# Kernel optimization log

Hardware: AMD Instinct MI355X
Metric: run time of the kernel (lower is better)

## Reference

```python
import jax, jax.numpy as jnp
import numpy as np

N = 50000          # neuron_count
NNZ = 1_600_000    # edges (avg degree 32)
B = 32             # batch
L = 3              # CONNECTOME_LAYER_NUMBER


def setup_inputs() -> dict:
    key = jax.random.key(0)
    k1, k2, k3, k4, k5 = jax.random.split(key, 5)
    x = jax.random.normal(k1, (B, N), dtype=jnp.float32)
    adj_vals = jax.random.uniform(k2, (NNZ,), dtype=jnp.float32)
    w_vals = jax.random.uniform(k3, (NNZ,), dtype=jnp.float32)
    bias = jnp.ones((N,), dtype=jnp.float32)
    row = jax.random.randint(k4, (NNZ,), 0, N, dtype=jnp.int32)
    col = jax.random.randint(k5, (NNZ,), 0, N, dtype=jnp.int32)
    return {"x": x, "adj_vals": adj_vals, "w_vals": w_vals, "bias": bias,
            "row": row, "col": col}


def _spmm(vals, row, col, dense, n):
    # (sparse NxN) @ dense [N, B] via gather + segment_sum scatter
    contrib = vals[:, None] * dense[col]          # [nnz, B]
    return jax.ops.segment_sum(contrib, row, num_segments=n)


def reference(x, adj_vals, w_vals, bias, row, col):
    # Original per layer: x = ((A @ W) @ x^T)^T + bias.
    # We use associativity: (A @ W) @ x^T == A @ (W @ x^T), avoiding the
    # explicit SpGEMM while computing the same linear map.
    n = bias.shape[0]
    xt = x.T                                      # [N, B]
    for _ in range(L):
        wx = _spmm(w_vals, row, col, xt, n)       # W @ x^T -> [N, B]
        xt = _spmm(adj_vals, row, col, wx, n)     # A @ (W @ x^T)
        xt = xt + bias[:, None]                   # broadcast bias over batch
    return xt.T                                   # [B, N]
```

## Files before the change

kernel.cpp:

```cpp
#include <hip/hip_runtime.h>


#define NN 50000
#define NNZ_E 1600000
#define NB (NN * 32)
#define CHUNK 6144
#define NBLK1 ((NNZ_E + CHUNK - 1) / CHUNK)
#define NBIN ((NN + 127) / 128)
#define NH (NBIN * NBLK1)
#define CAP2 5120
#define BCAP 6144
#define LENP (NBIN * BCAP)
#define SCAN_NBLK ((NH + 255) / 256)
#define TIN_BLKS 98

__device__ __forceinline__ int clampi(int v, int hi) {
    v = v < 0 ? 0 : v;
    return v > hi ? hi : v;
}

__device__ __forceinline__ unsigned short f2h(float v) {
    union { _Float16 h; unsigned short u; } cv;
    cv.h = (_Float16)v;
    return cv.u;
}

__device__ __forceinline__ float kv_val(unsigned kv) {
    union { unsigned short u; _Float16 h; } cv;
    cv.u = (unsigned short)(kv >> 16);
    return (float)cv.h;
}

__global__ __launch_bounds__(256) void hist_kernel(const int* __restrict__ row,
                                                   int* __restrict__ hist1,
                                                   const float* __restrict__ x,
                                                   _Float16* __restrict__ xt) {
    __shared__ int h[NBIN];
    int blk = blockIdx.x, tid = threadIdx.x;
    if (blk >= NBLK1) {
        for (int i = (blk - NBLK1) * 256 + tid; i < NB; i += TIN_BLKS * 256) {
            int n = i >> 5;
            int b = i & 31;
            xt[i] = (_Float16)x[b * NN + n];
        }
        return;
    }
    for (int j = tid; j < NBIN; j += 256) h[j] = 0;
    __syncthreads();
    int base = blk * CHUNK;
    int n = NNZ_E - base; if (n > CHUNK) n = CHUNK;
    for (int i = tid; i < n; i += 256)
        atomicAdd(&h[clampi(row[base + i], NN - 1) >> 7], 1);
    __syncthreads();
    for (int j = tid; j < NBIN; j += 256) hist1[j * NBLK1 + blk] = h[j];
}

__global__ void scan_local_kernel(int* __restrict__ data, int n, int* __restrict__ bsum) {
    __shared__ int s[256];
    int i = blockIdx.x * 256 + threadIdx.x;
    int v = (i < n) ? data[i] : 0;
    s[threadIdx.x] = v;
    __syncthreads();
    for (int off = 1; off < 256; off <<= 1) {
        int t = (threadIdx.x >= off) ? s[threadIdx.x - off] : 0;
        __syncthreads();
        s[threadIdx.x] += t;
        __syncthreads();
    }
    if (i < n) data[i] = s[threadIdx.x] - v;
    if (threadIdx.x == 255) bsum[blockIdx.x] = s[threadIdx.x];
}

__global__ __launch_bounds__(256) void scanfin_kernel(int* __restrict__ data, int n,
                                                      const int* __restrict__ bsum, int m,
                                                      int* __restrict__ binstart) {
    __shared__ int sa[512];
    __shared__ int sb[512];
    int tid = threadIdx.x;
    sa[tid]       = (tid < m) ? bsum[tid] : 0;
    sa[tid + 256] = (tid + 256 < m) ? bsum[tid + 256] : 0;
    __syncthreads();
    int* src = sa;
    int* dst = sb;
    for (int off = 1; off < 512; off <<= 1) {
#pragma unroll
        for (int q = 0; q < 2; ++q) {
            int p = tid + q * 256;
            int v = src[p];
            if (p >= off) v += src[p - off];
            dst[p] = v;
        }
        __syncthreads();
        int* t = src; src = dst; dst = t;
    }
    int add = (blockIdx.x > 0) ? src[blockIdx.x - 1] : 0;
    int i = blockIdx.x * 256 + tid;
    if (i < n) {
        int v = data[i] + add;
        data[i] = v;
        if (i % NBLK1 == 0) binstart[i / NBLK1] = v;
    }
    if (i == 0) binstart[NBIN] = NNZ_E;
}

__global__ __launch_bounds__(256) void pass1_kernel(
        const int* __restrict__ row, const int* __restrict__ col,
        const float* __restrict__ a, const float* __restrict__ w,
        const int* __restrict__ hist1_off,
        unsigned* __restrict__ k1, unsigned* __restrict__ aw1) {
    __shared__ int h[NBIN];
    __shared__ int hscan[NBIN];
    __shared__ int hoff[NBIN];
    __shared__ int s256[256];
    __shared__ unsigned sKey[CHUNK];
    __shared__ unsigned sAW[CHUNK];
    int blk = blockIdx.x, tid = threadIdx.x;
    int base = blk * CHUNK;
    int n = NNZ_E - base; if (n > CHUNK) n = CHUNK;

    for (int j = tid; j < NBIN; j += 256) {
        h[j] = 0;
        hoff[j] = hist1_off[j * NBLK1 + blk];
    }
    __syncthreads();
    for (int i = tid; i < n; i += 256)
        atomicAdd(&h[clampi(row[base + i], NN - 1) >> 7], 1);
    __syncthreads();
    int j0 = tid * 2, j1 = tid * 2 + 1;
    int c0 = (j0 < NBIN) ? h[j0] : 0;
    int c1 = (j1 < NBIN) ? h[j1] : 0;
    int tsum = c0 + c1;
    s256[tid] = tsum;
    __syncthreads();
    for (int off = 1; off < 256; off <<= 1) {
        int t = (tid >= off) ? s256[tid - off] : 0;
        __syncthreads();
        s256[tid] += t;
        __syncthreads();
    }
    int ex = s256[tid] - tsum;
    __syncthreads();
    if (j0 < NBIN) { hscan[j0] = ex;      h[j0] = ex; }
    if (j1 < NBIN) { hscan[j1] = ex + c0; h[j1] = ex + c0; }
    __syncthreads();
    for (int i = tid; i < n; i += 256) {
        int r = clampi(row[base + i], NN - 1);
        int c = clampi(col[base + i], NN - 1);
        int bin = r >> 7;
        int p = atomicAdd(&h[bin], 1);
        p = clampi(p, n - 1);
        sKey[p] = ((unsigned)r << 16) | (unsigned)c;
        sAW[p] = ((unsigned)f2h(a[base + i]) << 16) | (unsigned)f2h(w[base + i]);
    }
    __syncthreads();
    for (int p = tid; p < n; p += 256) {
        unsigned key = sKey[p];
        int bin = (int)(key >> 23);
        int d = clampi(hoff[bin] + (p - hscan[bin]), NNZ_E - 1);
        k1[d] = key;
        aw1[d] = sAW[p];
    }
}

__global__ __launch_bounds__(256) void pass2_kernel(
        const unsigned* __restrict__ k1, const unsigned* __restrict__ aw1,
        const int* __restrict__ binstart,
        unsigned* __restrict__ kvA2, unsigned* __restrict__ kvW2,
        unsigned* __restrict__ row_desc) {
    __shared__ unsigned sKey[CAP2];
    __shared__ unsigned sAW[CAP2];
    __shared__ int rh[128];
    __shared__ int rs[128];
    __shared__ int cur[128];
    int bin = blockIdx.x, tid = threadIdx.x;
    int r0 = bin << 7;
    int rows = NN - r0; if (rows > 128) rows = 128;
    int base = clampi(binstart[bin], NNZ_E);
    int size = clampi(binstart[bin + 1], NNZ_E) - base;
    size = clampi(size, CAP2);
    int pbase = bin * BCAP;

    if (tid < 128) rh[tid] = 0;
    __syncthreads();
    for (int i = tid; i < size; i += 256) {
        unsigned key = k1[base + i];
        atomicAdd(&rh[(key >> 16) & 127], 1);
        sKey[i] = key;
        sAW[i] = aw1[base + i];
    }
    __syncthreads();
    int cnt  = (tid < 128) ? rh[tid] : 0;
    int plen = (cnt + 7) & ~7;
    if (tid < 128) rs[tid] = plen;
    __syncthreads();
    for (int off = 1; off < 128; off <<= 1) {
        int t = (tid >= off && tid < 128) ? rs[tid - off] : 0;
        __syncthreads();
        if (tid < 128) rs[tid] += t;
        __syncthreads();
    }
    int rofs = (tid < 128) ? clampi(rs[tid] - plen, BCAP - 8) : 0;
    if (tid < 128) cur[tid] = rofs;
    if (tid < rows)
        row_desc[r0 + tid] = (unsigned)(pbase + rofs) | ((unsigned)(plen >> 3) << 24);
    __syncthreads();
    for (int i = tid; i < size; i += 256) {
        unsigned key = sKey[i];
        unsigned aw  = sAW[i];
        int rl = (key >> 16) & 127;
        int p = atomicAdd(&cur[rl], 1);
        p = clampi(p, BCAP - 1);
        unsigned c = key & 0xFFFFu;
        kvA2[pbase + p] = (aw & 0xFFFF0000u) | c;
        kvW2[pbase + p] = (aw << 16) | c;
    }
    __syncthreads();
    if (tid < rows) {
        int pl = (rh[tid] + 7) & ~7;
        for (int q = rh[tid]; q < pl; ++q) {
            int d = clampi(rofs + q, BCAP - 1);
            kvA2[pbase + d] = 0u;
            kvW2[pbase + d] = 0u;
        }
    }
}

template <int WITH_BIAS, int FINAL>
__global__ __launch_bounds__(256) void spmm_kernel(
        const uint2* __restrict__ kv2, const unsigned* __restrict__ row_desc,
        const unsigned* __restrict__ in32, unsigned* __restrict__ out32,
        const float* __restrict__ bias, float outScale, float biasScale,
        float* __restrict__ outf) {
    int t = blockIdx.x * 256 + threadIdx.x;
    int r = t >> 4;
    int l = t & 15;
    if (r >= NN) return;
    unsigned d = row_desc[r];
    int niter = (int)(d >> 24);
    int base2 = clampi((int)(d & 0xFFFFFFu), LENP - 8) >> 1;
    float accL = 0.0f, accH = 0.0f;
    uint2 k2[4];
    if (niter > 0) {
#pragma unroll
        for (int q = 0; q < 4; ++q) k2[q] = kv2[base2 + q];
    }
    for (int it = 0; it < niter; ++it) {
        unsigned k[8];
#pragma unroll
        for (int q = 0; q < 4; ++q) { k[2 * q] = k2[q].x; k[2 * q + 1] = k2[q].y; }
        unsigned gd[8];
#pragma unroll
        for (int j = 0; j < 8; ++j) gd[j] = in32[((k[j] & 0xFFFFu) << 4) + l];
        if (it + 1 < niter) {
            int nb2 = base2 + (it + 1) * 4;
#pragma unroll
            for (int q = 0; q < 4; ++q) k2[q] = kv2[nb2 + q];
        }
#pragma unroll
        for (int j = 0; j < 8; ++j) {
            float v = kv_val(k[j]);
            union { unsigned u; _Float16 h[2]; } cv;
            cv.u = gd[j];
            accL += v * (float)cv.h[0];
            accH += v * (float)cv.h[1];
        }
    }
    float rL = accL * outScale, rH = accH * outScale;
    if (WITH_BIAS) {
        float bb = bias[r] * biasScale;
        rL += bb; rH += bb;
    }
    if (FINAL) {
        outf[(2 * l) * NN + r]     = rL * 16777216.0f;
        outf[(2 * l + 1) * NN + r] = rH * 16777216.0f;
    } else {
        union { unsigned u; _Float16 h[2]; } o;
        o.h[0] = (_Float16)rL;
        o.h[1] = (_Float16)rH;
        out32[(r << 4) + l] = o.u;
    }
}

extern "C" void kernel_launch(void* const* d_in, const int* in_sizes, int n_in,
                              void* d_out, int out_size, void* d_ws, size_t ws_size,
                              hipStream_t stream) {
    const float* x        = (const float*)d_in[0];
    const float* adj_vals = (const float*)d_in[1];
    const float* w_vals   = (const float*)d_in[2];
    const float* bias     = (const float*)d_in[3];
    const int*   row      = (const int*)d_in[4];
    const int*   col      = (const int*)d_in[5];
    float* out = (float*)d_out;

    unsigned*  k1        = (unsigned*)d_ws;
    unsigned*  aw1       = k1 + NNZ_E;
    unsigned*  kvA2      = aw1 + NNZ_E;
    unsigned*  kvW2      = kvA2 + LENP;
    _Float16*  xt16      = (_Float16*)(kvW2 + LENP);
    _Float16*  tmp16     = xt16 + NB;
    int*   hist1         = (int*)(tmp16 + NB);
    int*   bsumB         = hist1 + NH;
    int*   binstart      = bsumB + 512;
    unsigned* row_desc   = (unsigned*)(binstart + NBIN + 8);

    const int BS = 256;
    const int grid_spmm = (NN * 16 + BS - 1) / BS;

    hist_kernel<<<NBLK1 + TIN_BLKS, BS, 0, stream>>>(row, hist1, x, xt16);
    scan_local_kernel<<<SCAN_NBLK, BS, 0, stream>>>(hist1, NH, bsumB);
    scanfin_kernel<<<SCAN_NBLK, BS, 0, stream>>>(hist1, NH, bsumB, SCAN_NBLK, binstart);

    pass1_kernel<<<NBLK1, BS, 0, stream>>>(row, col, adj_vals, w_vals,
                                           hist1, k1, aw1);
    pass2_kernel<<<NBIN, BS, 0, stream>>>(k1, aw1, binstart, kvA2, kvW2, row_desc);

    const uint2* kvA = (const uint2*)kvA2;
    const uint2* kvW = (const uint2*)kvW2;
    const unsigned* xt32  = (const unsigned*)xt16;
    unsigned*       xt32w = (unsigned*)xt16;
    const unsigned* tm32  = (const unsigned*)tmp16;
    unsigned*       tm32w = (unsigned*)tmp16;

    const float r256 = 1.0f / 256.0f;
    spmm_kernel<0, 0><<<grid_spmm, BS, 0, stream>>>(kvW, row_desc, xt32, tm32w,
                                                    nullptr, 1.0f, 0.0f, nullptr);
    spmm_kernel<1, 0><<<grid_spmm, BS, 0, stream>>>(kvA, row_desc, tm32, xt32w,
                                                    bias, r256, 1.0f / 256.0f, nullptr);
    spmm_kernel<0, 0><<<grid_spmm, BS, 0, stream>>>(kvW, row_desc, xt32, tm32w,
                                                    nullptr, 1.0f, 0.0f, nullptr);
    spmm_kernel<1, 0><<<grid_spmm, BS, 0, stream>>>(kvA, row_desc, tm32, xt32w,
                                                    bias, r256, 1.0f / 65536.0f, nullptr);
    spmm_kernel<0, 0><<<grid_spmm, BS, 0, stream>>>(kvW, row_desc, xt32, tm32w,
                                                    nullptr, 1.0f, 0.0f, nullptr);
    spmm_kernel<1, 1><<<grid_spmm, BS, 0, stream>>>(kvA, row_desc, tm32, xt32w,
                                                    bias, r256, 1.0f / 16777216.0f, out);
}
```

Baseline: 241.7 us.

## Replace two-pass binned sort with per-row histogram and atomic scatter CSR build

Replaces the two-level bin sort (per-chunk bin histograms, large scan, shared-memory local sort, then per-bin row sort) with a direct CSR build. The new build does a per-row global atomic histogram, a two-level row scan, and an atomic-cursor scatter of packed edges into padded per-row slots. Padding comes from zeroing the whole edge buffer up front. This cuts kernel count, scan size and the intermediate buffers, but relies on heavily contended global atomics and non-coalesced scattered writes. Edge order within a row also becomes nondeterministic.

```diff
diff --git a/kernel.cpp b/kernel.cpp
--- a/kernel.cpp
+++ b/kernel.cpp
@@ -4,15 +4,12 @@
 #define NN 50000
 #define NNZ_E 1600000
 #define NB (NN * 32)
-#define CHUNK 6144
-#define NBLK1 ((NNZ_E + CHUNK - 1) / CHUNK)
-#define NBIN ((NN + 127) / 128)
-#define NH (NBIN * NBLK1)
-#define CAP2 5120
-#define BCAP 6144
-#define LENP (NBIN * BCAP)
-#define SCAN_NBLK ((NH + 255) / 256)
+#define KVCAP 2097152
+#define NNP 50048
+#define ROW_NBLK ((NN + 255) / 256)
 #define TIN_BLKS 98
+#define ZBLKS 1024
+#define ZERO_U4 ((2 * KVCAP + 2 * NNP) / 4)
 
 __device__ __forceinline__ int clampi(int v, int hi) {
     v = v < 0 ? 0 : v;
@@ -31,198 +28,85 @@
     return (float)cv.h;
 }
 
-__global__ __launch_bounds__(256) void hist_kernel(const int* __restrict__ row,
-                                                   int* __restrict__ hist1,
+__global__ __launch_bounds__(256) void zero_kernel(uint4* __restrict__ z,
                                                    const float* __restrict__ x,
                                                    _Float16* __restrict__ xt) {
-    __shared__ int h[NBIN];
     int blk = blockIdx.x, tid = threadIdx.x;
-    if (blk >= NBLK1) {
-        for (int i = (blk - NBLK1) * 256 + tid; i < NB; i += TIN_BLKS * 256) {
+    if (blk >= ZBLKS) {
+        for (int i = (blk - ZBLKS) * 256 + tid; i < NB; i += TIN_BLKS * 256) {
             int n = i >> 5;
             int b = i & 31;
             xt[i] = (_Float16)x[b * NN + n];
         }
         return;
     }
-    for (int j = tid; j < NBIN; j += 256) h[j] = 0;
-    __syncthreads();
-    int base = blk * CHUNK;
-    int n = NNZ_E - base; if (n > CHUNK) n = CHUNK;
-    for (int i = tid; i < n; i += 256)
-        atomicAdd(&h[clampi(row[base + i], NN - 1) >> 7], 1);
-    __syncthreads();
-    for (int j = tid; j < NBIN; j += 256) hist1[j * NBLK1 + blk] = h[j];
-}
-
-__global__ void scan_local_kernel(int* __restrict__ data, int n, int* __restrict__ bsum) {
+    const uint4 zv = make_uint4(0u, 0u, 0u, 0u);
+    for (int i = blk * 256 + tid; i < ZERO_U4; i += ZBLKS * 256) z[i] = zv;
+}
+
+__global__ __launch_bounds__(256) void hist2_kernel(const int* __restrict__ row,
+                                                    int* __restrict__ rowcnt) {
+    int i = blockIdx.x * 256 + threadIdx.x;
+    if (i < NNZ_E) atomicAdd(&rowcnt[clampi(row[i], NN - 1)], 1);
+}
+
+__global__ __launch_bounds__(256) void scanrow_local_kernel(
+        const int* __restrict__ rowcnt, int* __restrict__ rowstart,
+        int* __restrict__ bsum) {
     __shared__ int s[256];
-    int i = blockIdx.x * 256 + threadIdx.x;
-    int v = (i < n) ? data[i] : 0;
-    s[threadIdx.x] = v;
+    int tid = threadIdx.x;
+    int i = blockIdx.x * 256 + tid;
+    int cnt = (i < NN) ? clampi(rowcnt[i], 2040) : 0;
+    int plen = (cnt + 7) & ~7;
+    s[tid] = plen;
     __syncthreads();
     for (int off = 1; off < 256; off <<= 1) {
-        int t = (threadIdx.x >= off) ? s[threadIdx.x - off] : 0;
-        __syncthreads();
-        s[threadIdx.x] += t;
-        __syncthreads();
-    }
-    if (i < n) data[i] = s[threadIdx.x] - v;
-    if (threadIdx.x == 255) bsum[blockIdx.x] = s[threadIdx.x];
-}
-
-__global__ __launch_bounds__(256) void scanfin_kernel(int* __restrict__ data, int n,
-                                                      const int* __restrict__ bsum, int m,
-                                                      int* __restrict__ binstart) {
-    __shared__ int sa[512];
-    __shared__ int sb[512];
+        int t = (tid >= off) ? s[tid - off] : 0;
+        __syncthreads();
+        s[tid] += t;
+        __syncthreads();
+    }
+    if (i < NN) rowstart[i] = s[tid] - plen;
+    if (tid == 255) bsum[blockIdx.x] = s[tid];
+}
+
+__global__ __launch_bounds__(256) void scanrow_fin_kernel(
+        const int* __restrict__ rowcnt, int* __restrict__ rowstart,
+        const int* __restrict__ bsum, unsigned* __restrict__ row_desc) {
+    __shared__ int s[256];
     int tid = threadIdx.x;
-    sa[tid]       = (tid < m) ? bsum[tid] : 0;
-    sa[tid + 256] = (tid + 256 < m) ? bsum[tid + 256] : 0;
+    s[tid] = (tid < ROW_NBLK) ? bsum[tid] : 0;
     __syncthreads();
-    int* src = sa;
-    int* dst = sb;
-    for (int off = 1; off < 512; off <<= 1) {
-#pragma unroll
-        for (int q = 0; q < 2; ++q) {
-            int p = tid + q * 256;
-            int v = src[p];
-            if (p >= off) v += src[p - off];
-            dst[p] = v;
-        }
-        __syncthreads();
-        int* t = src; src = dst; dst = t;
-    }
-    int add = (blockIdx.x > 0) ? src[blockIdx.x - 1] : 0;
+    for (int off = 1; off < 256; off <<= 1) {
+        int t = (tid >= off) ? s[tid - off] : 0;
+        __syncthreads();
+        s[tid] += t;
+        __syncthreads();
+    }
+    int add = (blockIdx.x > 0) ? s[blockIdx.x - 1] : 0;
     int i = blockIdx.x * 256 + tid;
-    if (i < n) {
-        int v = data[i] + add;
-        data[i] = v;
-        if (i % NBLK1 == 0) binstart[i / NBLK1] = v;
-    }
-    if (i == 0) binstart[NBIN] = NNZ_E;
-}
-
-__global__ __launch_bounds__(256) void pass1_kernel(
+    if (i < NN) {
+        int cnt = clampi(rowcnt[i], 2040);
+        int plen = (cnt + 7) & ~7;
+        int st = clampi(rowstart[i] + add, KVCAP - 8);
+        rowstart[i] = st;
+        row_desc[i] = (unsigned)st | ((unsigned)(plen >> 3) << 24);
+    }
+}
+
+__global__ __launch_bounds__(256) void scatter_kernel(
         const int* __restrict__ row, const int* __restrict__ col,
         const float* __restrict__ a, const float* __restrict__ w,
-        const int* __restrict__ hist1_off,
-        unsigned* __restrict__ k1, unsigned* __restrict__ aw1) {
-    __shared__ int h[NBIN];
-    __shared__ int hscan[NBIN];
-    __shared__ int hoff[NBIN];
-    __shared__ int s256[256];
-    __shared__ unsigned sKey[CHUNK];
-    __shared__ unsigned sAW[CHUNK];
-    int blk = blockIdx.x, tid = threadIdx.x;
-    int base = blk * CHUNK;
-    int n = NNZ_E - base; if (n > CHUNK) n = CHUNK;
-
-    for (int j = tid; j < NBIN; j += 256) {
-        h[j] = 0;
-        hoff[j] = hist1_off[j * NBLK1 + blk];
-    }
-    __syncthreads();
-    for (int i = tid; i < n; i += 256)
-        atomicAdd(&h[clampi(row[base + i], NN - 1) >> 7], 1);
-    __syncthreads();
-    int j0 = tid * 2, j1 = tid * 2 + 1;
-    int c0 = (j0 < NBIN) ? h[j0] : 0;
-    int c1 = (j1 < NBIN) ? h[j1] : 0;
-    int tsum = c0 + c1;
-    s256[tid] = tsum;
-    __syncthreads();
-    for (int off = 1; off < 256; off <<= 1) {
-        int t = (tid >= off) ? s256[tid - off] : 0;
-        __syncthreads();
-        s256[tid] += t;
-        __syncthreads();
-    }
-    int ex = s256[tid] - tsum;
-    __syncthreads();
-    if (j0 < NBIN) { hscan[j0] = ex;      h[j0] = ex; }
-    if (j1 < NBIN) { hscan[j1] = ex + c0; h[j1] = ex + c0; }
-    __syncthreads();
-    for (int i = tid; i < n; i += 256) {
-        int r = clampi(row[base + i], NN - 1);
-        int c = clampi(col[base + i], NN - 1);
-        int bin = r >> 7;
-        int p = atomicAdd(&h[bin], 1);
-        p = clampi(p, n - 1);
-        sKey[p] = ((unsigned)r << 16) | (unsigned)c;
-        sAW[p] = ((unsigned)f2h(a[base + i]) << 16) | (unsigned)f2h(w[base + i]);
-    }
-    __syncthreads();
-    for (int p = tid; p < n; p += 256) {
-        unsigned key = sKey[p];
-        int bin = (int)(key >> 23);
-        int d = clampi(hoff[bin] + (p - hscan[bin]), NNZ_E - 1);
-        k1[d] = key;
-        aw1[d] = sAW[p];
-    }
-}
-
-__global__ __launch_bounds__(256) void pass2_kernel(
-        const unsigned* __restrict__ k1, const unsigned* __restrict__ aw1,
-        const int* __restrict__ binstart,
-        unsigned* __restrict__ kvA2, unsigned* __restrict__ kvW2,
-        unsigned* __restrict__ row_desc) {
-    __shared__ unsigned sKey[CAP2];
-    __shared__ unsigned sAW[CAP2];
-    __shared__ int rh[128];
-    __shared__ int rs[128];
-    __shared__ int cur[128];
-    int bin = blockIdx.x, tid = threadIdx.x;
-    int r0 = bin << 7;
-    int rows = NN - r0; if (rows > 128) rows = 128;
-    int base = clampi(binstart[bin], NNZ_E);
-    int size = clampi(binstart[bin + 1], NNZ_E) - base;
-    size = clampi(size, CAP2);
-    int pbase = bin * BCAP;
-
-    if (tid < 128) rh[tid] = 0;
-    __syncthreads();
-    for (int i = tid; i < size; i += 256) {
-        unsigned key = k1[base + i];
-        atomicAdd(&rh[(key >> 16) & 127], 1);
-        sKey[i] = key;
-        sAW[i] = aw1[base + i];
-    }
-    __syncthreads();
-    int cnt  = (tid < 128) ? rh[tid] : 0;
-    int plen = (cnt + 7) & ~7;
-    if (tid < 128) rs[tid] = plen;
-    __syncthreads();
-    for (int off = 1; off < 128; off <<= 1) {
-        int t = (tid >= off && tid < 128) ? rs[tid - off] : 0;
-        __syncthreads();
-        if (tid < 128) rs[tid] += t;
-        __syncthreads();
-    }
-    int rofs = (tid < 128) ? clampi(rs[tid] - plen, BCAP - 8) : 0;
-    if (tid < 128) cur[tid] = rofs;
-    if (tid < rows)
-        row_desc[r0 + tid] = (unsigned)(pbase + rofs) | ((unsigned)(plen >> 3) << 24);
-    __syncthreads();
-    for (int i = tid; i < size; i += 256) {
-        unsigned key = sKey[i];
-        unsigned aw  = sAW[i];
-        int rl = (key >> 16) & 127;
-        int p = atomicAdd(&cur[rl], 1);
-        p = clampi(p, BCAP - 1);
-        unsigned c = key & 0xFFFFu;
-        kvA2[pbase + p] = (aw & 0xFFFF0000u) | c;
-        kvW2[pbase + p] = (aw << 16) | c;
-    }
-    __syncthreads();
-    if (tid < rows) {
-        int pl = (rh[tid] + 7) & ~7;
-        for (int q = rh[tid]; q < pl; ++q) {
-            int d = clampi(rofs + q, BCAP - 1);
-            kvA2[pbase + d] = 0u;
-            kvW2[pbase + d] = 0u;
-        }
-    }
+        const int* __restrict__ rowstart, int* __restrict__ cnt2,
+        unsigned* __restrict__ kvA2, unsigned* __restrict__ kvW2) {
+    int i = blockIdx.x * 256 + threadIdx.x;
+    if (i >= NNZ_E) return;
+    int r = clampi(row[i], NN - 1);
+    int c = clampi(col[i], NN - 1);
+    int q = atomicAdd(&cnt2[r], 1);
+    int p = clampi(rowstart[r] + q, KVCAP - 1);
+    kvA2[p] = ((unsigned)f2h(a[i]) << 16) | (unsigned)c;
+    kvW2[p] = ((unsigned)f2h(w[i]) << 16) | (unsigned)c;
 }
 
 template <int WITH_BIAS, int FINAL>
@@ -237,7 +121,7 @@
     if (r >= NN) return;
     unsigned d = row_desc[r];
     int niter = (int)(d >> 24);
-    int base2 = clampi((int)(d & 0xFFFFFFu), LENP - 8) >> 1;
+    int base2 = clampi((int)(d & 0xFFFFFFu), KVCAP - 8) >> 1;
     float accL = 0.0f, accH = 0.0f;
     uint2 k2[4];
     if (niter > 0) {
@@ -292,27 +176,26 @@
     const int*   col      = (const int*)d_in[5];
     float* out = (float*)d_out;
 
-    unsigned*  k1        = (unsigned*)d_ws;
-    unsigned*  aw1       = k1 + NNZ_E;
-    unsigned*  kvA2      = aw1 + NNZ_E;
-    unsigned*  kvW2      = kvA2 + LENP;
-    _Float16*  xt16      = (_Float16*)(kvW2 + LENP);
+    unsigned*  kvA2      = (unsigned*)d_ws;
+    unsigned*  kvW2      = kvA2 + KVCAP;
+    int*       rowcnt    = (int*)(kvW2 + KVCAP);
+    int*       cnt2      = rowcnt + NNP;
+    int*       rowstart  = cnt2 + NNP;
+    int*       bsum      = rowstart + NNP;
+    unsigned*  row_desc  = (unsigned*)(bsum + 256);
+    _Float16*  xt16      = (_Float16*)(row_desc + NN + 8);
     _Float16*  tmp16     = xt16 + NB;
-    int*   hist1         = (int*)(tmp16 + NB);
-    int*   bsumB         = hist1 + NH;
-    int*   binstart      = bsumB + 512;
-    unsigned* row_desc   = (unsigned*)(binstart + NBIN + 8);
 
     const int BS = 256;
-    const int grid_spmm = (NN * 16 + BS - 1) / BS;
-
-    hist_kernel<<<NBLK1 + TIN_BLKS, BS, 0, stream>>>(row, hist1, x, xt16);
-    scan_local_kernel<<<SCAN_NBLK, BS, 0, stream>>>(hist1, NH, bsumB);
-    scanfin_kernel<<<SCAN_NBLK, BS, 0, stream>>>(hist1, NH, bsumB, SCAN_NBLK, binstart);
-
-    pass1_kernel<<<NBLK1, BS, 0, stream>>>(row, col, adj_vals, w_vals,
-                                           hist1, k1, aw1);
-    pass2_kernel<<<NBIN, BS, 0, stream>>>(k1, aw1, binstart, kvA2, kvW2, row_desc);
+    const int grid_edges = (NNZ_E + BS - 1) / BS;
+    const int grid_spmm  = (NN * 16 + BS - 1) / BS;
+
+    zero_kernel<<<ZBLKS + TIN_BLKS, BS, 0, stream>>>((uint4*)d_ws, x, xt16);
+    hist2_kernel<<<grid_edges, BS, 0, stream>>>(row, rowcnt);
+    scanrow_local_kernel<<<ROW_NBLK, BS, 0, stream>>>(rowcnt, rowstart, bsum);
+    scanrow_fin_kernel<<<ROW_NBLK, BS, 0, stream>>>(rowcnt, rowstart, bsum, row_desc);
+    scatter_kernel<<<grid_edges, BS, 0, stream>>>(row, col, adj_vals, w_vals,
+                                                  rowstart, cnt2, kvA2, kvW2);
 
     const uint2* kvA = (const uint2*)kvA2;
     const uint2* kvW = (const uint2*)kvW2;
```

After: 407.7 us. 1.69x slower.
